# Kernel tuning notes

Measured on AMD Instinct MI355X. Metric: run time of the kernel, lower is better.

The kernel has to match this reference:

```python
import jax, jax.numpy as jnp
import numpy as np

SHAPE = (4, 16, 16)          # (t, h, w) latent shape
E, H, L = 576, 16, 6         # embd_dim, n_head, n_layer
DK = E // H                  # head dim = 36
SEQ = int(np.prod(SHAPE))    # 1024
B = 2


def _layernorm(x, s, b):
    m = x.mean(-1, keepdims=True)
    v = ((x - m) ** 2).mean(-1, keepdims=True)
    return (x - m) * jax.lax.rsqrt(v + 1e-5) * s + b


def _masks():
    # causal lower-triangular mask and L1 distance-decay mask (FullAttention.__init__)
    causal = np.tril(np.ones((SEQ, SEQ), dtype=bool))
    grids = np.meshgrid(*[np.arange(s) for s in SHAPE], indexing='ij')
    coords = np.stack([g.ravel() for g in grids], -1)          # [SEQ, 3]
    dist = np.abs(coords[:, None, :] - coords[None, :, :]).sum(-1).astype(np.float32)
    dm = np.exp(-dist / dist[0, -1])                            # max distance = dist[0, SEQ-1]
    return jnp.asarray(causal), jnp.asarray(dm)


def setup_inputs() -> dict:
    key = jax.random.key(0)
    ks = jax.random.split(key, 12)
    f32 = jnp.float32
    std = 1.0 / np.sqrt(E)
    pe = E // 3
    d = {}
    d['x'] = jax.random.normal(ks[0], (B, *SHAPE, E), f32)
    d['sos'] = jax.random.normal(ks[1], (E,), f32) * 0.02
    d['pe0'] = jax.random.normal(ks[2], (SHAPE[0], pe), f32) * 0.01
    d['pe1'] = jax.random.normal(ks[3], (SHAPE[1], pe), f32) * 0.01
    d['pe2'] = jax.random.normal(ks[4], (SHAPE[2], pe), f32) * 0.01
    d['ln1_s'] = jnp.ones((L, E), f32); d['ln1_b'] = jnp.zeros((L, E), f32)
    d['wq'] = jax.random.normal(ks[5], (L, E, E), f32) * std
    d['wk'] = jax.random.normal(ks[6], (L, E, E), f32) * std
    d['wv'] = jax.random.normal(ks[7], (L, E, E), f32) * std
    d['wo'] = jax.random.normal(ks[8], (L, E, E), f32) * (1.0 / np.sqrt(E * L))
    d['bo'] = jnp.zeros((L, E), f32)
    d['ln2_s'] = jnp.ones((L, E), f32); d['ln2_b'] = jnp.zeros((L, E), f32)
    d['w1'] = jax.random.normal(ks[9], (L, E, 4 * E), f32) * std
    d['b1'] = jnp.zeros((L, 4 * E), f32)
    d['w2'] = jax.random.normal(ks[10], (L, 4 * E, E), f32) * (1.0 / np.sqrt(4 * E))
    d['b2'] = jnp.zeros((L, E), f32)
    return d


def _forward(x, sos, pe0, pe1, pe2, ln1_s, ln1_b, wq, wk, wv, wo, bo,
             ln2_s, ln2_b, w1, b1, w2, b2):
    b = x.shape[0]
    causal, dm = _masks()
    h = x.reshape(b, SEQ, E)
    # RightShift: prepend learned SOS token, drop last
    h = jnp.concatenate([jnp.broadcast_to(sos, (b, 1, E)), h[:, :-1]], axis=1)
    # AddBroadcastPosEmbed (dim=-1): per-axis embeddings concatenated on channels
    pos = jnp.concatenate([
        jnp.broadcast_to(pe0[:, None, None, :], (*SHAPE, E // 3)),
        jnp.broadcast_to(pe1[None, :, None, :], (*SHAPE, E // 3)),
        jnp.broadcast_to(pe2[None, None, :, :], (*SHAPE, E // 3)),
    ], axis=-1).reshape(SEQ, E)
    h = h + pos
    scale = 1.0 / np.sqrt(DK)
    for l in range(L):  # fixed small layer loop
        y = _layernorm(h, ln1_s[l], ln1_b[l])
        q = (y @ wq[l]).reshape(b, SEQ, H, DK).transpose(0, 2, 1, 3)
        k = (y @ wk[l]).reshape(b, SEQ, H, DK).transpose(0, 2, 1, 3)
        v = (y @ wv[l]).reshape(b, SEQ, H, DK).transpose(0, 2, 1, 3)
        s = jnp.einsum('bhqd,bhkd->bhqk', q, k) * scale
        s = s * dm                              # elementwise distance-decay mask
        s = jnp.where(causal, s, -jnp.inf)       # causal masked_fill
        a = jax.nn.softmax(s, axis=-1)
        o = jnp.einsum('bhqk,bhkd->bhqd', a, v)
        o = o.transpose(0, 2, 1, 3).reshape(b, SEQ, E) @ wo[l] + bo[l]
        h = h + o
        y = _layernorm(h, ln2_s[l], ln2_b[l])
        y1 = y @ w1[l] + b1[l]
        y1 = jax.nn.sigmoid(1.702 * y1) * y1     # GeLU2
        h = h + (y1 @ w2[l] + b2[l])
    return h.reshape(b, *SHAPE, E)


def reference(x, sos, pe0, pe1, pe2, ln1_s, ln1_b, wq, wk, wv, wo, bo,
              ln2_s, ln2_b, w1, b1, w2, b2):
    return _forward(x, sos, pe0, pe1, pe2, ln1_s, ln1_b, wq, wk, wv, wo, bo,
                    ln2_s, ln2_b, w1, b1, w2, b2)
```

## Files before the change

kernel.cpp:

```cpp
#include <hip/hip_runtime.h>


#define E_    576
#define SEQ_  1024
#define B_    2
#define NH_   16
#define DK_   36
#define DKP_  64
#define NL_   6
#define FF_   2304
#define ROWS_ 2048

typedef unsigned short u16;
typedef unsigned int u32;
typedef float f32x4 __attribute__((ext_vector_type(4)));
typedef __bf16 bf16x8 __attribute__((ext_vector_type(8)));
typedef __bf16 bf16x4 __attribute__((ext_vector_type(4)));

#define MFMA16(a, b, c) __builtin_amdgcn_mfma_f32_16x16x32_bf16((a), (b), (c), 0, 0, 0)

__device__ __forceinline__ float bf2f(u16 u) {
    return __uint_as_float(((unsigned)u) << 16);
}
__device__ __forceinline__ u16 f2bf(float f) {
    unsigned u = __float_as_uint(f);
    u += 0x7fffu + ((u >> 16) & 1u);
    return (u16)(u >> 16);
}
__device__ __forceinline__ float load_in(const void* p, size_t i, int isf32) {
    return isf32 ? ((const float*)p)[i] : bf2f(((const u16*)p)[i]);
}
__device__ __forceinline__ u16 load_in_bf(const void* p, size_t i, int isf32) {
    return isf32 ? f2bf(((const float*)p)[i]) : ((const u16*)p)[i];
}
__device__ __forceinline__ bf16x8 ldg8(const u16* p) {
    uint4 u = *(const uint4*)p;
    bf16x8 r;
    __builtin_memcpy(&r, &u, 16);
    return r;
}
__device__ __forceinline__ void gload_lds16(const u16* g, u16* l) {
    __builtin_amdgcn_global_load_lds(
        (const __attribute__((address_space(1))) unsigned int*)g,
        (__attribute__((address_space(3))) unsigned int*)l, 16, 0, 0);
}

__global__ void detect_kernel(const u16* __restrict__ x, int* __restrict__ flag)
{
    __shared__ float red[4];
    int lane = threadIdx.x & 63, wave = threadIdx.x >> 6;
    float mx = 0.f;
    for (int i = threadIdx.x; i < 4096; i += 256) {
        float v = fabsf(bf2f(x[i]));
        if (v < 3e38f) mx = fmaxf(mx, v);
    }
    for (int off = 1; off < 64; off <<= 1) mx = fmaxf(mx, __shfl_xor(mx, off));
    if (lane == 0) red[wave] = mx;
    __syncthreads();
    if (threadIdx.x == 0) {
        float m = fmaxf(fmaxf(red[0], red[1]), fmaxf(red[2], red[3]));
        *flag = (m > 1e6f) ? 1 : 0;
    }
}

__global__ __launch_bounds__(256) void repack_kernel(
    const void* __restrict__ wq, const void* __restrict__ wk,
    const void* __restrict__ wv, const void* __restrict__ wo,
    const void* __restrict__ w1, const void* __restrict__ w2,
    u16* __restrict__ wT, const int* __restrict__ flagp)
{
    __shared__ u32 tile[64 * 33];
    int isf32 = *flagp;
    int idx = blockIdx.x, l = blockIdx.z;
    const void* src;
    u16* dst;
    size_t sbase;
    int R, C, cx, ry;
    if (idx < 324) {
        int t4 = idx / 81, rem = idx - t4 * 81;
        ry = rem / 9; cx = rem % 9; R = 576; C = 576;
        src = (t4 == 0) ? wq : (t4 == 1) ? wk : (t4 == 2) ? wv : wo;
        sbase = (size_t)l * 331776;
        dst = wT + (size_t)l * 3981312 + t4 * 331776;
    } else if (idx < 648) {
        int rem = idx - 324;
        ry = rem / 36; cx = rem % 36; R = 576; C = 2304;
        src = w1; sbase = (size_t)l * 1327104;
        dst = wT + (size_t)l * 3981312 + 1327104;
    } else {
        int rem = idx - 648;
        ry = rem / 9; cx = rem % 9; R = 2304; C = 576;
        src = w2; sbase = (size_t)l * 1327104;
        dst = wT + (size_t)l * 3981312 + 2654208;
    }
    int r0 = ry * 64, c0 = cx * 64;
    int t = threadIdx.x;
    int chunk = t & 15, row = t >> 4;
    #pragma unroll
    for (int i = 0; i < 4; i++) {
        int rr = row + i * 16;
        size_t g = sbase + (size_t)(r0 + rr) * C + c0 + chunk * 4;
        u32 lo, hi;
        if (isf32) {
            f32x4 v = *(const f32x4*)((const float*)src + g);
            lo = (u32)f2bf(v[0]) | ((u32)f2bf(v[1]) << 16);
            hi = (u32)f2bf(v[2]) | ((u32)f2bf(v[3]) << 16);
        } else {
            uint2 v = *(const uint2*)((const u16*)src + g);
            lo = v.x; hi = v.y;
        }
        tile[rr * 33 + chunk * 2] = lo;
        tile[rr * 33 + chunk * 2 + 1] = hi;
    }
    __syncthreads();
    int p = t & 31, nl = t >> 5;
    #pragma unroll
    for (int i = 0; i < 8; i++) {
        int nn = nl + i * 8;
        u32 wA = tile[(2 * p) * 33 + (nn >> 1)];
        u32 wB = tile[(2 * p + 1) * 33 + (nn >> 1)];
        u32 a = (nn & 1) ? (wA >> 16) : (wA & 0xffffu);
        u32 b = (nn & 1) ? (wB >> 16) : (wB & 0xffffu);
        u32* d32 = (u32*)(dst + (size_t)(c0 + nn) * R + r0);
        d32[p] = a | (b << 16);
    }
}

__global__ void embed_kernel(
    const void* __restrict__ x, const void* __restrict__ sos,
    const void* __restrict__ pe0, const void* __restrict__ pe1,
    const void* __restrict__ pe2, float* __restrict__ h,
    const int* __restrict__ flagp)
{
    int isf32 = *flagp;
    int row = blockIdx.x;
    int e = threadIdx.x;
    int s = row & 1023;
    float v = (s == 0) ? load_in(sos, e, isf32)
                       : load_in(x, (size_t)(row - 1) * E_ + e, isf32);
    int t = s >> 8, hh = (s >> 4) & 15, ww = s & 15;
    float p = (e < 192) ? load_in(pe0, t * 192 + e, isf32)
            : (e < 384) ? load_in(pe1, hh * 192 + e - 192, isf32)
                        : load_in(pe2, ww * 192 + e - 384, isf32);
    h[(size_t)row * E_ + e] = v + p;
}

__global__ __launch_bounds__(256) void ln_kernel(
    const float* __restrict__ h, u16* __restrict__ y,
    const void* __restrict__ sc, const void* __restrict__ bi,
    int off0, const int* __restrict__ flagp)
{
    int isf32 = *flagp;
    int lane = threadIdx.x & 63, wave = threadIdx.x >> 6;
    int row = blockIdx.x * 4 + wave;
    const float* hr = h + (size_t)row * E_;
    float v[9], s = 0.f, sq = 0.f;
    for (int j = 0; j < 9; j++) {
        v[j] = hr[lane + j * 64];
        s += v[j];
        sq += v[j] * v[j];
    }
    for (int off = 1; off < 64; off <<= 1) {
        s += __shfl_xor(s, off);
        sq += __shfl_xor(sq, off);
    }
    float mean = s * (1.0f / E_);
    float var = sq * (1.0f / E_) - mean * mean;
    float r = rsqrtf(var + 1e-5f);
    for (int j = 0; j < 9; j++) {
        int e = lane + j * 64;
        float sce = load_in(sc, off0 + e, isf32);
        float bie = load_in(bi, off0 + e, isf32);
        y[(size_t)row * E_ + e] = f2bf((v[j] - mean) * r * sce + bie);
    }
}

template <int MODE, int SPLITK>
__global__ __launch_bounds__(256) void gemm_kernel(
    const u16* __restrict__ A, const u16* __restrict__ BtBase, int K,
    const void* __restrict__ bias, int boff, float* __restrict__ hbuf,
    u16* __restrict__ out, u16* __restrict__ qb, u16* __restrict__ kb,
    u16* __restrict__ vtb, const int* __restrict__ flagp)
{
    __shared__ u16 lA[8192];
    __shared__ u16 lB[4096];
    int t = threadIdx.x;
    int lane = t & 63, wave = t >> 6;
    int lw = lane & 15, lq = lane >> 4;
    int wx = wave >> 1, wy = wave & 1;
    int m0 = blockIdx.x * 128, n0 = blockIdx.y * 64;
    int z = blockIdx.z / SPLITK, kz = blockIdx.z % SPLITK;
    int Ks = K / SPLITK, kbase = kz * Ks;

    const u16* Bt = BtBase + (MODE == 0 ? (size_t)z * 331776 : 0);
    int rowS = t >> 3;
    int gc = (t & 7) ^ (rowS & 7);
    const u16* gA = A + (size_t)(m0 + rowS) * K + kbase + gc * 8;
    const u16* gB = Bt + (size_t)(n0 + rowS) * K + kbase + gc * 8;
    size_t rstep = (size_t)32 * K;

    f32x4 acc[4][2];
    for (int mi = 0; mi < 4; mi++)
        for (int ni = 0; ni < 2; ni++)
            for (int r = 0; r < 4; r++) acc[mi][ni][r] = 0.f;

    for (int kc = 0; kc < Ks; kc += 64) {
        #pragma unroll
        for (int ra = 0; ra < 4; ra++)
            gload_lds16(gA + ra * rstep + kc, &lA[ra * 2048 + t * 8]);
        #pragma unroll
        for (int rb = 0; rb < 2; rb++)
            gload_lds16(gB + rb * rstep + kc, &lB[rb * 2048 + t * 8]);
        __syncthreads();
        #pragma unroll
        for (int ks = 0; ks < 2; ks++) {
            int csw = ((ks * 4 + lq) ^ (lw & 7)) * 8;
            bf16x8 bf0 = ldg8(&lB[(wy * 32 + lw) * 64 + csw]);
            bf16x8 bf1 = ldg8(&lB[(wy * 32 + 16 + lw) * 64 + csw]);
            #pragma unroll
            for (int mi = 0; mi < 4; mi++) {
                bf16x8 af = ldg8(&lA[(wx * 64 + mi * 16 + lw) * 64 + csw]);
                acc[mi][0] = MFMA16(af, bf0, acc[mi][0]);
                acc[mi][1] = MFMA16(af, bf1, acc[mi][1]);
            }
        }
        __syncthreads();
    }

    int isf32 = (MODE != 0) ? *flagp : 0;
    #pragma unroll
    for (int ni = 0; ni < 2; ni++) {
        int n = n0 + wy * 32 + ni * 16 + lw;
        float bn = 0.f;
        if (MODE == 2 || ((MODE == 1 || MODE == 3) && kz == 0))
            bn = load_in(bias, boff + n, isf32);
        #pragma unroll
        for (int mi = 0; mi < 4; mi++) {
            #pragma unroll
            for (int r = 0; r < 4; r++) {
                int m = m0 + wx * 64 + mi * 16 + lq * 4 + r;
                float v = acc[mi][ni][r];
                if (MODE == 0) {
                    int b = m >> 10, s = m & 1023;
                    int head = n / 36, d = n - head * 36;
                    size_t bh = (size_t)(b * NH_ + head);
                    if (z == 0)
                        qb[(bh * SEQ_ + s) * DKP_ + d] = f2bf(v * (1.0f / 6.0f));
                    else if (z == 1)
                        kb[(bh * SEQ_ + s) * DKP_ + d] = f2bf(v);
                    else
                        vtb[(bh * DKP_ + d) * SEQ_ + s] = f2bf(v);
                } else if (MODE == 2) {
                    float tt = v + bn;
                    out[(size_t)m * FF_ + n] = f2bf(tt / (1.0f + __expf(-1.702f * tt)));
                } else {
                    atomicAdd(&hbuf[(size_t)m * E_ + n], v + bn);
                }
            }
        }
    }
}

__global__ __launch_bounds__(256, 4) void attn_kernel(
    const u16* __restrict__ qb, const u16* __restrict__ kb,
    const u16* __restrict__ vtb, u16* __restrict__ ob)
{
    __shared__ float sm[4][16], sl[4][16], so[4][16][52];
    int lane = threadIdx.x & 63, wave = threadIdx.x >> 6;
    int lw = lane & 15, lq = lane >> 4;
    int L = blockIdx.x;
    int bh = L & 31;
    int qt = 63 - (L >> 5);
    int head = bh & 15, b = bh >> 4;
    int q0 = qt * 16;

    const u16* qrow = qb + ((size_t)bh * SEQ_ + q0 + lw) * DKP_ + lq * 8;
    bf16x8 qf0 = ldg8(qrow);
    bf16x8 qf1 = ldg8(qrow + 32);

    int tq = q0 >> 8, hq = (q0 >> 4) & 15;
    int qg = q0 + lw;
    int wq8 = (lq & 1) * 8;
    float ew8[8];
    #pragma unroll
    for (int i = 0; i < 8; i++)
        ew8[i] = __expf((float)abs(lw - (wq8 + i)) * (-1.0f / 33.0f));

    float m_i = -1e30f, l_i = 0.f;
    f32x4 oacc[3];
    #pragma unroll
    for (int c2 = 0; c2 < 3; c2++)
        #pragma unroll
        for (int r = 0; r < 4; r++) oacc[c2][r] = 0.f;

    int kperm = (lw >> 2) * 8 + (lw & 3);
    const u16* kbh = kb + (size_t)bh * SEQ_ * DKP_;
    const u16* vbh = vtb + (size_t)bh * DKP_ * SEQ_;

    int nch = (q0 >> 6) + 1;
    for (int c = wave; c < nch; c += 4) {
        int kv0 = c * 64;
        bf16x8 kf[4][2], vf[3][2];
        #pragma unroll
        for (int kvh = 0; kvh < 4; kvh++) {
            const u16* kp = kbh +
                (size_t)(kv0 + (kvh >> 1) * 32 + (kvh & 1) * 4 + kperm) * DKP_
                + lq * 8;
            kf[kvh][0] = ldg8(kp);
            kf[kvh][1] = ldg8(kp + 32);
        }
        #pragma unroll
        for (int c2 = 0; c2 < 3; c2++) {
            const u16* vp = vbh + (size_t)(c2 * 16 + lw) * SEQ_ + kv0 + lq * 8;
            vf[c2][0] = ldg8(vp);
            vf[c2][1] = ldg8(vp + 32);
        }
        f32x4 st[4];
        #pragma unroll
        for (int kvh = 0; kvh < 4; kvh++) {
            f32x4 tt;
            #pragma unroll
            for (int r = 0; r < 4; r++) tt[r] = 0.f;
            tt = MFMA16(kf[kvh][0], qf0, tt);
            tt = MFMA16(kf[kvh][1], qf1, tt);
            st[kvh] = tt;
        }
        int tk = kv0 >> 8, hk0 = (kv0 >> 4) & 15;
        float sB[4];
        #pragma unroll
        for (int i = 0; i < 4; i++)
            sB[i] = __expf((float)(abs(tq - tk) + abs(hq - hk0 - i))
                           * (-1.0f / 33.0f));
        float fh0 = sB[lq >> 1], fh1 = sB[(lq >> 1) + 2];
        float vv[4][4];
        #pragma unroll
        for (int kvh = 0; kvh < 4; kvh++) {
            float fh = (kvh < 2) ? fh0 : fh1;
            #pragma unroll
            for (int r = 0; r < 4; r++)
                vv[kvh][r] = st[kvh][r] * (fh * ew8[(kvh & 1) * 4 + r]);
        }
        if (c == nch - 1) {
            #pragma unroll
            for (int kvh = 0; kvh < 4; kvh++) {
                int koff = kv0 + (kvh >> 1) * 32 + lq * 8 + (kvh & 1) * 4;
                #pragma unroll
                for (int r = 0; r < 4; r++)
                    if (koff + r > qg) vv[kvh][r] = -1e30f;
            }
        }
        float mloc =
            fmaxf(fmaxf(fmaxf(fmaxf(vv[0][0], vv[0][1]), fmaxf(vv[0][2], vv[0][3])),
                        fmaxf(fmaxf(vv[1][0], vv[1][1]), fmaxf(vv[1][2], vv[1][3]))),
                  fmaxf(fmaxf(fmaxf(vv[2][0], vv[2][1]), fmaxf(vv[2][2], vv[2][3])),
                        fmaxf(fmaxf(vv[3][0], vv[3][1]), fmaxf(vv[3][2], vv[3][3]))));
        mloc = fmaxf(mloc, __shfl_xor(mloc, 16));
        mloc = fmaxf(mloc, __shfl_xor(mloc, 32));
        float mn = fmaxf(m_i, mloc);
        float alpha = __expf(m_i - mn);
        m_i = mn;
        float p[4][4];
        float rs = 0.f;
        #pragma unroll
        for (int kvh = 0; kvh < 4; kvh++) {
            #pragma unroll
            for (int r = 0; r < 4; r++) {
                p[kvh][r] = __expf(vv[kvh][r] - mn);
                rs += p[kvh][r];
            }
        }
        rs += __shfl_xor(rs, 16);
        rs += __shfl_xor(rs, 32);
        l_i = l_i * alpha + rs;
        #pragma unroll
        for (int c2 = 0; c2 < 3; c2++)
            #pragma unroll
            for (int r = 0; r < 4; r++) oacc[c2][r] *= alpha;
        bf16x8 pf0, pf1;
        #pragma unroll
        for (int r = 0; r < 4; r++) {
            pf0[r]     = (__bf16)p[0][r];
            pf0[4 + r] = (__bf16)p[1][r];
            pf1[r]     = (__bf16)p[2][r];
            pf1[4 + r] = (__bf16)p[3][r];
        }
        #pragma unroll
        for (int c2 = 0; c2 < 3; c2++) {
            oacc[c2] = MFMA16(vf[c2][0], pf0, oacc[c2]);
            oacc[c2] = MFMA16(vf[c2][1], pf1, oacc[c2]);
        }
    }

    if (lq == 0) { sm[wave][lw] = m_i; sl[wave][lw] = l_i; }
    #pragma unroll
    for (int c2 = 0; c2 < 3; c2++)
        #pragma unroll
        for (int r = 0; r < 4; r++)
            so[wave][lw][c2 * 16 + lq * 4 + r] = oacc[c2][r];
    __syncthreads();
    for (int i = threadIdx.x; i < 16 * DK_; i += 256) {
        int row = i / DK_, col = i - row * DK_;
        float M = fmaxf(fmaxf(sm[0][row], sm[1][row]),
                        fmaxf(sm[2][row], sm[3][row]));
        float Lm = 0.f, O = 0.f;
        #pragma unroll
        for (int w = 0; w < 4; w++) {
            float f = __expf(sm[w][row] - M);
            Lm += f * sl[w][row];
            O += f * so[w][row][col];
        }
        ob[((size_t)b * SEQ_ + q0 + row) * E_ + head * DK_ + col] = f2bf(O / Lm);
    }
}

__global__ void out_kernel(const float* __restrict__ h, void* __restrict__ out,
                           const int* __restrict__ flagp)
{
    int isf32 = *flagp;
    int i = blockIdx.x * blockDim.x + threadIdx.x;
    if (isf32) ((float*)out)[i] = h[i];
    else       ((u16*)out)[i] = f2bf(h[i]);
}

extern "C" void kernel_launch(void* const* d_in, const int* in_sizes, int n_in,
                              void* d_out, int out_size, void* d_ws,
                              size_t ws_size, hipStream_t stream)
{
    const void* x    = d_in[0];
    const void* sos  = d_in[1];
    const void* pe0  = d_in[2];
    const void* pe1  = d_in[3];
    const void* pe2  = d_in[4];
    const void* ln1s = d_in[5];
    const void* ln1b = d_in[6];
    const void* wq   = d_in[7];
    const void* wk   = d_in[8];
    const void* wv   = d_in[9];
    const void* wo   = d_in[10];
    const void* bo   = d_in[11];
    const void* ln2s = d_in[12];
    const void* ln2b = d_in[13];
    const void* w1   = d_in[14];
    const void* b1   = d_in[15];
    const void* w2   = d_in[16];
    const void* b2   = d_in[17];

    char* ws = (char*)d_ws;
    u16*   qbuf  = (u16*)(ws + 0);
    u16*   kbuf  = (u16*)(ws + 4194304);
    u16*   vtbuf = (u16*)(ws + 8388608);
    float* h     = (float*)(ws + 12582912);
    u16*   y     = (u16*)(ws + 17301504);
    u16*   o     = (u16*)(ws + 19660800);
    u16*   y1    = (u16*)(ws + 22020096);
    u16*   wT    = (u16*)(ws + 31457280);
    int*   flag  = (int*)(ws + 79233024);

    hipMemsetAsync(ws, 0, 12582912, stream);
    detect_kernel<<<1, 256, 0, stream>>>((const u16*)x, flag);
    repack_kernel<<<dim3(972, 1, 6), 256, 0, stream>>>(
        wq, wk, wv, wo, w1, w2, wT, flag);
    embed_kernel<<<ROWS_, E_, 0, stream>>>(x, sos, pe0, pe1, pe2, h, flag);

    for (int l = 0; l < NL_; l++) {
        u16* wTl = wT + (size_t)l * 3981312;
        ln_kernel<<<512, 256, 0, stream>>>(h, y, ln1s, ln1b, l * E_, flag);
        gemm_kernel<0, 1><<<dim3(16, 9, 3), 256, 0, stream>>>(
            y, wTl, E_, nullptr, 0, nullptr, nullptr, qbuf, kbuf, vtbuf, flag);
        attn_kernel<<<dim3(2048), 256, 0, stream>>>(qbuf, kbuf, vtbuf, o);
        gemm_kernel<1, 3><<<dim3(16, 9, 3), 256, 0, stream>>>(
            o, wTl + 995328, E_, bo, l * E_, h, nullptr, nullptr, nullptr, nullptr, flag);
        ln_kernel<<<512, 256, 0, stream>>>(h, y, ln2s, ln2b, l * E_, flag);
        gemm_kernel<2, 1><<<dim3(16, 36, 1), 256, 0, stream>>>(
            y, wTl + 1327104, E_, b1, l * FF_, nullptr, y1, nullptr, nullptr, nullptr, flag);
        gemm_kernel<3, 4><<<dim3(16, 9, 4), 256, 0, stream>>>(
            y1, wTl + 2654208, FF_, b2, l * E_, h, nullptr, nullptr, nullptr, nullptr, flag);
    }
    out_kernel<<<4608, 256, 0, stream>>>(h, d_out, flag);
}
```

Baseline: 846.5 us.

## Double-buffer GEMM LDS tiles to overlap global loads with MFMA

Doubles the shared-memory A/B tiles and prefetches the next K chunk into the alternate buffer while the current one is consumed by MFMAs. A single combined vmcnt wait and barrier per iteration replaces the two syncthreads. The aim is to hide global-to-LDS load latency. In exchange LDS use per block doubles to 48KB, which may lower occupancy. The barrier placement also needs care: it relies on s_barrier ordering the LDS reads of one buffer before the next iteration overwrites it.

```diff
diff --git a/kernel.cpp b/kernel.cpp
--- a/kernel.cpp
+++ b/kernel.cpp
@@ -18,6 +18,8 @@
 typedef __bf16 bf16x4 __attribute__((ext_vector_type(4)));
 
 #define MFMA16(a, b, c) __builtin_amdgcn_mfma_f32_16x16x32_bf16((a), (b), (c), 0, 0, 0)
+
+#define VMBAR() asm volatile("s_waitcnt vmcnt(0)\n\ts_barrier" ::: "memory")
 
 __device__ __forceinline__ float bf2f(u16 u) {
     return __uint_as_float(((unsigned)u) << 16);
@@ -182,8 +184,8 @@
     u16* __restrict__ out, u16* __restrict__ qb, u16* __restrict__ kb,
     u16* __restrict__ vtb, const int* __restrict__ flagp)
 {
-    __shared__ u16 lA[8192];
-    __shared__ u16 lB[4096];
+    __shared__ u16 lA[2][8192];
+    __shared__ u16 lB[2][4096];
     int t = threadIdx.x;
     int lane = t & 63, wave = t >> 6;
     int lw = lane & 15, lq = lane >> 4;
@@ -204,28 +206,39 @@
         for (int ni = 0; ni < 2; ni++)
             for (int r = 0; r < 4; r++) acc[mi][ni][r] = 0.f;
 
-    for (int kc = 0; kc < Ks; kc += 64) {
+    auto stage = [&](int buf, int kc) {
         #pragma unroll
         for (int ra = 0; ra < 4; ra++)
-            gload_lds16(gA + ra * rstep + kc, &lA[ra * 2048 + t * 8]);
+            gload_lds16(gA + ra * rstep + kc, &lA[buf][ra * 2048 + t * 8]);
         #pragma unroll
         for (int rb = 0; rb < 2; rb++)
-            gload_lds16(gB + rb * rstep + kc, &lB[rb * 2048 + t * 8]);
-        __syncthreads();
+            gload_lds16(gB + rb * rstep + kc, &lB[buf][rb * 2048 + t * 8]);
+    };
+    auto compute = [&](int buf) {
         #pragma unroll
         for (int ks = 0; ks < 2; ks++) {
             int csw = ((ks * 4 + lq) ^ (lw & 7)) * 8;
-            bf16x8 bf0 = ldg8(&lB[(wy * 32 + lw) * 64 + csw]);
-            bf16x8 bf1 = ldg8(&lB[(wy * 32 + 16 + lw) * 64 + csw]);
+            bf16x8 bf0 = ldg8(&lB[buf][(wy * 32 + lw) * 64 + csw]);
+            bf16x8 bf1 = ldg8(&lB[buf][(wy * 32 + 16 + lw) * 64 + csw]);
             #pragma unroll
             for (int mi = 0; mi < 4; mi++) {
-                bf16x8 af = ldg8(&lA[(wx * 64 + mi * 16 + lw) * 64 + csw]);
+                bf16x8 af = ldg8(&lA[buf][(wx * 64 + mi * 16 + lw) * 64 + csw]);
                 acc[mi][0] = MFMA16(af, bf0, acc[mi][0]);
                 acc[mi][1] = MFMA16(af, bf1, acc[mi][1]);
             }
         }
-        __syncthreads();
-    }
+    };
+
+    stage(0, 0);
+    VMBAR();
+    int cur = 0;
+    for (int kc = 0; kc + 64 < Ks; kc += 64) {
+        stage(cur ^ 1, kc + 64);
+        compute(cur);
+        VMBAR();
+        cur ^= 1;
+    }
+    compute(cur);
 
     int isf32 = (MODE != 0) ? *flagp : 0;
     #pragma unroll
```

Result: slower. 882.8 us (+4.3%).

## Replace split-K atomic accumulation with partial buffers reduced inside layernorm

Applied to the files above, without the earlier changes.

Split-K GEMMs for the attention output and MLP down-projection now write per-split partial sums to separate workspace buffers instead of atomically adding into the residual. The following layernorm kernel (and the final output kernel) sums the residual with the partials, writes back the updated residual, and then normalises. This removes float atomic contention in the GEMM epilogue. In exchange it adds extra global reads and writes of the partial buffers and needs more workspace.

```diff
diff --git a/kernel.cpp b/kernel.cpp
--- a/kernel.cpp
+++ b/kernel.cpp
@@ -10,6 +10,7 @@
 #define NL_   6
 #define FF_   2304
 #define ROWS_ 2048
+#define PSTRIDE_ 1179648
 
 typedef unsigned short u16;
 typedef unsigned int u32;
@@ -29,9 +30,6 @@
 }
 __device__ __forceinline__ float load_in(const void* p, size_t i, int isf32) {
     return isf32 ? ((const float*)p)[i] : bf2f(((const u16*)p)[i]);
-}
-__device__ __forceinline__ u16 load_in_bf(const void* p, size_t i, int isf32) {
-    return isf32 ? f2bf(((const float*)p)[i]) : ((const u16*)p)[i];
 }
 __device__ __forceinline__ bf16x8 ldg8(const u16* p) {
     uint4 u = *(const uint4*)p;
@@ -145,20 +143,29 @@
     h[(size_t)row * E_ + e] = v + p;
 }
 
+template <int NPART>
 __global__ __launch_bounds__(256) void ln_kernel(
-    const float* __restrict__ h, u16* __restrict__ y,
+    float* __restrict__ h, u16* __restrict__ y,
+    const float* __restrict__ parts,
     const void* __restrict__ sc, const void* __restrict__ bi,
     int off0, const int* __restrict__ flagp)
 {
     int isf32 = *flagp;
     int lane = threadIdx.x & 63, wave = threadIdx.x >> 6;
     int row = blockIdx.x * 4 + wave;
-    const float* hr = h + (size_t)row * E_;
+    float* hr = h + (size_t)row * E_;
     float v[9], s = 0.f, sq = 0.f;
+    #pragma unroll
     for (int j = 0; j < 9; j++) {
-        v[j] = hr[lane + j * 64];
-        s += v[j];
-        sq += v[j] * v[j];
+        int e = lane + j * 64;
+        float t = hr[e];
+        #pragma unroll
+        for (int pk = 0; pk < NPART; pk++)
+            t += parts[(size_t)pk * PSTRIDE_ + (size_t)row * E_ + e];
+        if (NPART > 0) hr[e] = t;
+        v[j] = t;
+        s += t;
+        sq += t * t;
     }
     for (int off = 1; off < 64; off <<= 1) {
         s += __shfl_xor(s, off);
@@ -167,6 +174,7 @@
     float mean = s * (1.0f / E_);
     float var = sq * (1.0f / E_) - mean * mean;
     float r = rsqrtf(var + 1e-5f);
+    #pragma unroll
     for (int j = 0; j < 9; j++) {
         int e = lane + j * 64;
         float sce = load_in(sc, off0 + e, isf32);
@@ -178,7 +186,7 @@
 template <int MODE, int SPLITK>
 __global__ __launch_bounds__(256) void gemm_kernel(
     const u16* __restrict__ A, const u16* __restrict__ BtBase, int K,
-    const void* __restrict__ bias, int boff, float* __restrict__ hbuf,
+    const void* __restrict__ bias, int boff, float* __restrict__ pout,
     u16* __restrict__ out, u16* __restrict__ qb, u16* __restrict__ kb,
     u16* __restrict__ vtb, const int* __restrict__ flagp)
 {
@@ -254,7 +262,7 @@
                     float tt = v + bn;
                     out[(size_t)m * FF_ + n] = f2bf(tt / (1.0f + __expf(-1.702f * tt)));
                 } else {
-                    atomicAdd(&hbuf[(size_t)m * E_ + n], v + bn);
+                    pout[(size_t)kz * PSTRIDE_ + (size_t)m * E_ + n] = v + bn;
                 }
             }
         }
@@ -413,13 +421,17 @@
     }
 }
 
-__global__ void out_kernel(const float* __restrict__ h, void* __restrict__ out,
+__global__ void out_kernel(const float* __restrict__ h,
+                           const float* __restrict__ p3,
+                           void* __restrict__ out,
                            const int* __restrict__ flagp)
 {
     int isf32 = *flagp;
-    int i = blockIdx.x * blockDim.x + threadIdx.x;
-    if (isf32) ((float*)out)[i] = h[i];
-    else       ((u16*)out)[i] = f2bf(h[i]);
+    size_t i = (size_t)blockIdx.x * blockDim.x + threadIdx.x;
+    float v = h[i] + p3[i] + p3[i + PSTRIDE_] + p3[i + 2 * PSTRIDE_]
+            + p3[i + 3 * PSTRIDE_];
+    if (isf32) ((float*)out)[i] = v;
+    else       ((u16*)out)[i] = f2bf(v);
 }
 
 extern "C" void kernel_launch(void* const* d_in, const int* in_sizes, int n_in,
@@ -455,6 +467,8 @@
     u16*   y1    = (u16*)(ws + 22020096);
     u16*   wT    = (u16*)(ws + 31457280);
     int*   flag  = (int*)(ws + 79233024);
+    float* p1    = (float*)(ws + 83886080);
+    float* p3    = (float*)(ws + 100663296);
 
     hipMemsetAsync(ws, 0, 12582912, stream);
     detect_kernel<<<1, 256, 0, stream>>>((const u16*)x, flag);
@@ -464,17 +478,23 @@
 
     for (int l = 0; l < NL_; l++) {
         u16* wTl = wT + (size_t)l * 3981312;
-        ln_kernel<<<512, 256, 0, stream>>>(h, y, ln1s, ln1b, l * E_, flag);
+        if (l == 0)
+            ln_kernel<0><<<512, 256, 0, stream>>>(h, y, nullptr, ln1s, ln1b,
+                                                  l * E_, flag);
+        else
+            ln_kernel<4><<<512, 256, 0, stream>>>(h, y, p3, ln1s, ln1b,
+                                                  l * E_, flag);
         gemm_kernel<0, 1><<<dim3(16, 9, 3), 256, 0, stream>>>(
             y, wTl, E_, nullptr, 0, nullptr, nullptr, qbuf, kbuf, vtbuf, flag);
         attn_kernel<<<dim3(2048), 256, 0, stream>>>(qbuf, kbuf, vtbuf, o);
         gemm_kernel<1, 3><<<dim3(16, 9, 3), 256, 0, stream>>>(
-            o, wTl + 995328, E_, bo, l * E_, h, nullptr, nullptr, nullptr, nullptr, flag);
-        ln_kernel<<<512, 256, 0, stream>>>(h, y, ln2s, ln2b, l * E_, flag);
+            o, wTl + 995328, E_, bo, l * E_, p1, nullptr, nullptr, nullptr, nullptr, flag);
+        ln_kernel<3><<<512, 256, 0, stream>>>(h, y, p1, ln2s, ln2b,
+                                              l * E_, flag);
         gemm_kernel<2, 1><<<dim3(16, 36, 1), 256, 0, stream>>>(
             y, wTl + 1327104, E_, b1, l * FF_, nullptr, y1, nullptr, nullptr, nullptr, flag);
         gemm_kernel<3, 4><<<dim3(16, 9, 4), 256, 0, stream>>>(
-            y1, wTl + 2654208, FF_, b2, l * E_, h, nullptr, nullptr, nullptr, nullptr, flag);
-    }
-    out_kernel<<<4608, 256, 0, stream>>>(h, d_out, flag);
-}
+            y1, wTl + 2654208, FF_, b2, l * E_, p3, nullptr, nullptr, nullptr, nullptr, flag);
+    }
+    out_kernel<<<4608, 256, 0, stream>>>(h, p3, d_out, flag);
+}
```

New measurement: 772.8 us. -8.7%, faster.
